# Kernel optimization log

Measured on AMD Instinct MI355X. Metric: run time of the kernel, lower is better.

## Reference

```python
import jax, jax.numpy as jnp
import numpy as np

N = 50000
E = 800000
IN_C, HID_C, OUT_C = 512, 128, 256


def setup_inputs() -> dict:
    key = jax.random.key(0)
    k1, k2, k3, k4, k5, k6 = jax.random.split(key, 6)
    x = jax.random.normal(k1, (N, IN_C), dtype=jnp.float32)
    edge_index = jax.random.randint(k2, (2, E), 0, N, dtype=jnp.int64)
    # Linear weights stored torch-style as [out, in]; bias per layer
    w1 = jax.random.normal(k3, (HID_C, IN_C), dtype=jnp.float32) * (1.0 / np.sqrt(IN_C))
    b1 = jax.random.normal(k4, (HID_C,), dtype=jnp.float32) * 0.02
    w2 = jax.random.normal(k5, (OUT_C, HID_C), dtype=jnp.float32) * (1.0 / np.sqrt(HID_C))
    b2 = jax.random.normal(k6, (OUT_C,), dtype=jnp.float32) * 0.02
    return {"x": x, "edge_index": edge_index, "w1": w1, "b1": b1, "w2": w2, "b2": b2}


def gcn_conv(x, edge_index, w, b):
    # x: [N, Cin], w: [Cout, Cin] (torch Linear layout), b: [Cout]
    h = x @ w.T                              # [N, Cout]
    src, dst = edge_index[0], edge_index[1]
    msgs = h[src]                            # gather: [E, Cout]
    agg = jax.ops.segment_sum(msgs, dst, num_segments=h.shape[0])  # scatter_add
    return agg + b


def reference(x, edge_index, w1, b1, w2, b2):
    h = gcn_conv(x, edge_index, w1, b1)
    h = jax.nn.relu(h)
    out = gcn_conv(h, edge_index, w2, b2)
    return out
```

## Files before the change

### kernel.cpp

```cpp
#include <hip/hip_runtime.h>

#define NN 50000
#define EE 800000
#define INC 512
#define HIDC 128
#define OUTC 256
#define CAP 64
#define OV_CAP 65536
#define BUILD_BLOCKS 192
#define BLK_PER_XCD (BUILD_BLOCKS / 8)
#define GRP_THREADS (BLK_PER_XCD * 256)
#define NCHUNK (EE / 16)
#define SLICE (NN / 8)
#define GB1 782

typedef __attribute__((ext_vector_type(8))) short bf16x8;
typedef __attribute__((ext_vector_type(4))) float f32x4;

__device__ __forceinline__ short f2bf(float f) {
    unsigned u = __float_as_uint(f);
    unsigned r = u + 0x7fff + ((u >> 16) & 1);
    return (short)(r >> 16);
}
__device__ __forceinline__ float bf2f(short s) {
    return __uint_as_float(((unsigned)(unsigned short)s) << 16);
}

template<bool IN_BF16, bool ADDBIAS, bool OUT_BF16>
__device__ __forceinline__ void gemm_core(
    const void* __restrict__ Av, const float* __restrict__ B,
    const float* __restrict__ bias, void* __restrict__ Cv,
    int M, int Nc, int K, int bx, int by,
    short As[64][72], short Bs[128][72])
{
    int tid = threadIdx.x;
    int lane = tid & 63, wave = tid >> 6;
    int row0 = bx * 64, col0 = by * 128;
    int wm = (wave & 1) * 32, wn = (wave >> 1) * 64;
    int l16 = lane & 15, quad = lane >> 4;

    f32x4 acc[2][4];
#pragma unroll
    for (int i = 0; i < 2; i++)
#pragma unroll
        for (int j = 0; j < 4; j++) acc[i][j] = {0.f, 0.f, 0.f, 0.f};

    for (int k0 = 0; k0 < K; k0 += 64) {
        if (IN_BF16) {
            const short* A = (const short*)Av;
#pragma unroll
            for (int w = 0; w < 2; w++) {
                int f = tid + w * 256;
                int rr = f >> 3, c8 = f & 7;
                int gr = row0 + rr;
                bf16x8 v = {0, 0, 0, 0, 0, 0, 0, 0};
                if (gr < M) v = *(const bf16x8*)&A[(long)gr * K + k0 + c8 * 8];
                *(bf16x8*)&As[rr][c8 * 8] = v;
            }
        } else {
            const float* A = (const float*)Av;
#pragma unroll
            for (int w = 0; w < 4; w++) {
                int f = tid + w * 256;
                int rr = f >> 4, c4 = f & 15;
                int gr = row0 + rr;
                float4 v = make_float4(0.f, 0.f, 0.f, 0.f);
                if (gr < M) v = *(const float4*)&A[(long)gr * K + k0 + c4 * 4];
                short4 s;
                s.x = f2bf(v.x); s.y = f2bf(v.y); s.z = f2bf(v.z); s.w = f2bf(v.w);
                *(short4*)&As[rr][c4 * 4] = s;
            }
        }
#pragma unroll
        for (int w = 0; w < 8; w++) {
            int f = tid + w * 256;
            int rr = f >> 4, c4 = f & 15;
            float4 v = *(const float4*)&B[(long)(col0 + rr) * K + k0 + c4 * 4];
            short4 s;
            s.x = f2bf(v.x); s.y = f2bf(v.y); s.z = f2bf(v.z); s.w = f2bf(v.w);
            *(short4*)&Bs[rr][c4 * 4] = s;
        }
        __syncthreads();

#pragma unroll
        for (int kk = 0; kk < 64; kk += 32) {
            bf16x8 af[2], bfr[4];
#pragma unroll
            for (int i = 0; i < 2; i++)
                af[i] = *(const bf16x8*)&As[wm + i * 16 + l16][kk + quad * 8];
#pragma unroll
            for (int j = 0; j < 4; j++)
                bfr[j] = *(const bf16x8*)&Bs[wn + j * 16 + l16][kk + quad * 8];
#pragma unroll
            for (int i = 0; i < 2; i++)
#pragma unroll
                for (int j = 0; j < 4; j++)
                    acc[i][j] = __builtin_amdgcn_mfma_f32_16x16x32_bf16(
                        af[i], bfr[j], acc[i][j], 0, 0, 0);
        }
        __syncthreads();
    }

#pragma unroll
    for (int i = 0; i < 2; i++) {
#pragma unroll
        for (int rr = 0; rr < 4; rr++) {
            int grow = row0 + wm + i * 16 + quad * 4 + rr;
            if (grow < M) {
#pragma unroll
                for (int j = 0; j < 4; j++) {
                    int gcol = col0 + wn + j * 16 + l16;
                    float v = acc[i][j][rr];
                    if (ADDBIAS) v += bias[gcol];
                    if (OUT_BF16)
                        ((short*)Cv)[(long)grow * Nc + gcol] = f2bf(v);
                    else
                        ((float*)Cv)[(long)grow * Nc + gcol] = v;
                }
            }
        }
    }
}

__global__ __launch_bounds__(256) void fat_build_gemm1(
    const int* __restrict__ ei, int* __restrict__ cnt,
    unsigned short* __restrict__ bucket, int* __restrict__ ovcnt,
    int* __restrict__ ovlist,
    const float* __restrict__ x, const float* __restrict__ w1,
    short* __restrict__ h)
{
    __shared__ short As[64][72];
    __shared__ short Bs[128][72];

    if (blockIdx.x < BUILD_BLOCKS) {
        int g = blockIdx.x & 7;
        int rank = blockIdx.x >> 3;
        int tig = rank * 256 + threadIdx.x;
        int lo = g * SLICE;
        for (int c = tig; c < NCHUNK; c += GRP_THREADS) {
            long base = (long)c * 16;
            int4 sv[4], dv[4];
#pragma unroll
            for (int q = 0; q < 4; q++) {
                sv[q] = *(const int4*)&ei[base + q * 4];
                dv[q] = *(const int4*)&ei[EE + base + q * 4];
            }
            const int* sp = (const int*)sv;
            const int* dp = (const int*)dv;
#pragma unroll
            for (int k = 0; k < 16; k++) {
                int dst = dp[k];
                if ((unsigned)(dst - lo) < SLICE) {
                    int src = sp[k];
                    int pos = atomicAdd(&cnt[dst], 1);
                    if (pos < CAP) bucket[(long)dst * CAP + pos] = (unsigned short)src;
                    else {
                        int o = atomicAdd(ovcnt, 1);
                        if (o < OV_CAP) { ovlist[o * 2] = src; ovlist[o * 2 + 1] = dst; }
                    }
                }
            }
        }
    } else {
        gemm_core<false, false, true>(x, w1, nullptr, h, NN, HIDC, INC,
                                      blockIdx.x - BUILD_BLOCKS, 0, As, Bs);
    }
}

__global__ __launch_bounds__(256) void gemm2_k(
    const short* __restrict__ r2, const float* __restrict__ w2,
    const float* __restrict__ b2, float* __restrict__ out)
{
    __shared__ short As[64][72];
    __shared__ short Bs[128][72];
    gemm_core<true, true, false>(r2, w2, b2, out, NN, OUTC, HIDC,
                                 blockIdx.x, blockIdx.y, As, Bs);
}

template<bool RELU>
__global__ __launch_bounds__(256) void gather_k(
    const short* __restrict__ hsrc, const unsigned short* __restrict__ bucket,
    const int* __restrict__ cnt, const float* __restrict__ bias,
    short* __restrict__ rout)
{
    int t = threadIdx.x;
    int node = blockIdx.x * 16 + (t >> 4);
    int c8 = t & 15;
    if (node >= NN) return;
    int m = cnt[node]; if (m > CAP) m = CAP;
    const unsigned short* bk = bucket + (long)node * CAP;
    float acc[8];
#pragma unroll
    for (int k = 0; k < 8; k++) acc[k] = 0.f;
    int j = 0;
    for (; j + 4 <= m; j += 4) {
        int s0 = bk[j], s1 = bk[j + 1], s2 = bk[j + 2], s3 = bk[j + 3];
        bf16x8 v0 = *(const bf16x8*)&hsrc[((long)s0 << 7) + c8 * 8];
        bf16x8 v1 = *(const bf16x8*)&hsrc[((long)s1 << 7) + c8 * 8];
        bf16x8 v2 = *(const bf16x8*)&hsrc[((long)s2 << 7) + c8 * 8];
        bf16x8 v3 = *(const bf16x8*)&hsrc[((long)s3 << 7) + c8 * 8];
#pragma unroll
        for (int k = 0; k < 8; k++)
            acc[k] += bf2f(v0[k]) + bf2f(v1[k]) + bf2f(v2[k]) + bf2f(v3[k]);
    }
    for (; j < m; j++) {
        int s0 = bk[j];
        bf16x8 v0 = *(const bf16x8*)&hsrc[((long)s0 << 7) + c8 * 8];
#pragma unroll
        for (int k = 0; k < 8; k++) acc[k] += bf2f(v0[k]);
    }
    bf16x8 o;
    if (RELU) {
#pragma unroll
        for (int k = 0; k < 8; k++)
            o[k] = f2bf(fmaxf(acc[k] + bias[c8 * 8 + k], 0.f));
    } else {
#pragma unroll
        for (int k = 0; k < 8; k++) o[k] = f2bf(acc[k]);
    }
    *(bf16x8*)&rout[((long)node << 7) + c8 * 8] = o;
}

__global__ __launch_bounds__(128) void ovfix1_k(
    const short* __restrict__ h, const float* __restrict__ b1,
    const unsigned short* __restrict__ bucket, const int* __restrict__ cnt,
    const int* __restrict__ ovcnt, const int* __restrict__ ovlist,
    short* __restrict__ r)
{
    int n = *ovcnt; if (n > OV_CAP) n = OV_CAP;
    int c = threadIdx.x;
    for (int i = 0; i < n; i++) {
        int dst = ovlist[i * 2 + 1];
        bool dup = false;
        for (int i2 = 0; i2 < i; i2++)
            if (ovlist[i2 * 2 + 1] == dst) { dup = true; break; }
        if (dup) continue;
        int m = cnt[dst]; if (m > CAP) m = CAP;
        const unsigned short* bk = bucket + (long)dst * CAP;
        float acc = 0.f;
        for (int j = 0; j < m; j++)
            acc += bf2f(h[(long)bk[j] * 128 + c]);
        for (int i2 = 0; i2 < n; i2++)
            if (ovlist[i2 * 2 + 1] == dst)
                acc += bf2f(h[(long)ovlist[i2 * 2] * 128 + c]);
        r[(long)dst * 128 + c] = f2bf(fmaxf(acc + b1[c], 0.f));
    }
}

__global__ __launch_bounds__(128) void ovfix2_k(
    const short* __restrict__ r, const unsigned short* __restrict__ bucket,
    const int* __restrict__ cnt, const int* __restrict__ ovcnt,
    const int* __restrict__ ovlist, short* __restrict__ r2)
{
    int n = *ovcnt; if (n > OV_CAP) n = OV_CAP;
    int c = threadIdx.x;
    for (int i = 0; i < n; i++) {
        int dst = ovlist[i * 2 + 1];
        bool dup = false;
        for (int i2 = 0; i2 < i; i2++)
            if (ovlist[i2 * 2 + 1] == dst) { dup = true; break; }
        if (dup) continue;
        int m = cnt[dst]; if (m > CAP) m = CAP;
        const unsigned short* bk = bucket + (long)dst * CAP;
        float acc = 0.f;
        for (int j = 0; j < m; j++)
            acc += bf2f(r[(long)bk[j] * 128 + c]);
        for (int i2 = 0; i2 < n; i2++)
            if (ovlist[i2 * 2 + 1] == dst)
                acc += bf2f(r[(long)ovlist[i2 * 2] * 128 + c]);
        r2[(long)dst * 128 + c] = f2bf(acc);
    }
}

extern "C" void kernel_launch(void* const* d_in, const int* in_sizes, int n_in,
                              void* d_out, int out_size, void* d_ws, size_t ws_size,
                              hipStream_t stream) {
    const float* x  = (const float*)d_in[0];
    const int*   ei = (const int*)d_in[1];
    const float* w1 = (const float*)d_in[2];
    const float* b1 = (const float*)d_in[3];
    const float* w2 = (const float*)d_in[4];
    const float* b2 = (const float*)d_in[5];
    float* out = (float*)d_out;

    char* ws = (char*)d_ws;
    size_t off = 0;
    short* h    = (short*)(ws + off); off += (size_t)NN * HIDC * 2;
    short* r    = (short*)(ws + off); off += (size_t)NN * HIDC * 2;
    short* r2   = (short*)(ws + off); off += (size_t)NN * HIDC * 2;
    unsigned short* bucket = (unsigned short*)(ws + off);
    off += (size_t)NN * CAP * 2;
    int* cnt    = (int*)(ws + off);   off += (size_t)NN * 4;
    int* ovcnt  = (int*)(ws + off);   off += 256;
    int* ovlist = (int*)(ws + off);   off += (size_t)OV_CAP * 2 * 4;

    hipMemsetAsync(cnt, 0, (size_t)NN * 4 + 4, stream);

    dim3 blk(256);

    fat_build_gemm1<<<dim3(BUILD_BLOCKS + GB1), blk, 0, stream>>>(
        ei, cnt, bucket, ovcnt, ovlist, x, w1, h);

    gather_k<true><<<dim3(3125), blk, 0, stream>>>(h, bucket, cnt, b1, r);
    ovfix1_k<<<dim3(1), dim3(128), 0, stream>>>(h, b1, bucket, cnt, ovcnt, ovlist, r);

    gather_k<false><<<dim3(3125), blk, 0, stream>>>(r, bucket, cnt, nullptr, r2);
    ovfix2_k<<<dim3(1), dim3(128), 0, stream>>>(r, bucket, cnt, ovcnt, ovlist, r2);

    gemm2_k<<<dim3(GB1, 2), blk, 0, stream>>>(r2, w2, b2, out);
}
```

Measured before the change: 329.6 us.

## Drop XCD-sliced edge bucketing and unroll gather loop to eight neighbors

```diff
diff --git a/kernel.cpp b/kernel.cpp
--- a/kernel.cpp
+++ b/kernel.cpp
@@ -7,11 +7,7 @@
 #define OUTC 256
 #define CAP 64
 #define OV_CAP 65536
-#define BUILD_BLOCKS 192
-#define BLK_PER_XCD (BUILD_BLOCKS / 8)
-#define GRP_THREADS (BLK_PER_XCD * 256)
-#define NCHUNK (EE / 16)
-#define SLICE (NN / 8)
+#define BUILD_BLOCKS 196
 #define GB1 782
 
 typedef __attribute__((ext_vector_type(8))) short bf16x8;
@@ -133,12 +129,9 @@
     __shared__ short Bs[128][72];
 
     if (blockIdx.x < BUILD_BLOCKS) {
-        int g = blockIdx.x & 7;
-        int rank = blockIdx.x >> 3;
-        int tig = rank * 256 + threadIdx.x;
-        int lo = g * SLICE;
-        for (int c = tig; c < NCHUNK; c += GRP_THREADS) {
-            long base = (long)c * 16;
+        int t = threadIdx.x;
+        long base = ((long)blockIdx.x * 256 + t) * 16;
+        if (base + 16 <= EE) {
             int4 sv[4], dv[4];
 #pragma unroll
             for (int q = 0; q < 4; q++) {
@@ -149,9 +142,19 @@
             const int* dp = (const int*)dv;
 #pragma unroll
             for (int k = 0; k < 16; k++) {
-                int dst = dp[k];
-                if ((unsigned)(dst - lo) < SLICE) {
-                    int src = sp[k];
+                int src = sp[k], dst = dp[k];
+                int pos = atomicAdd(&cnt[dst], 1);
+                if (pos < CAP) bucket[(long)dst * CAP + pos] = (unsigned short)src;
+                else {
+                    int o = atomicAdd(ovcnt, 1);
+                    if (o < OV_CAP) { ovlist[o * 2] = src; ovlist[o * 2 + 1] = dst; }
+                }
+            }
+        } else {
+            for (int k = 0; k < 16; k++) {
+                long e = base + k;
+                if (e < EE) {
+                    int src = ei[e], dst = ei[EE + e];
                     int pos = atomicAdd(&cnt[dst], 1);
                     if (pos < CAP) bucket[(long)dst * CAP + pos] = (unsigned short)src;
                     else {
@@ -193,15 +196,18 @@
 #pragma unroll
     for (int k = 0; k < 8; k++) acc[k] = 0.f;
     int j = 0;
-    for (; j + 4 <= m; j += 4) {
-        int s0 = bk[j], s1 = bk[j + 1], s2 = bk[j + 2], s3 = bk[j + 3];
-        bf16x8 v0 = *(const bf16x8*)&hsrc[((long)s0 << 7) + c8 * 8];
-        bf16x8 v1 = *(const bf16x8*)&hsrc[((long)s1 << 7) + c8 * 8];
-        bf16x8 v2 = *(const bf16x8*)&hsrc[((long)s2 << 7) + c8 * 8];
-        bf16x8 v3 = *(const bf16x8*)&hsrc[((long)s3 << 7) + c8 * 8];
-#pragma unroll
-        for (int k = 0; k < 8; k++)
-            acc[k] += bf2f(v0[k]) + bf2f(v1[k]) + bf2f(v2[k]) + bf2f(v3[k]);
+    for (; j + 8 <= m; j += 8) {
+        int s[8];
+#pragma unroll
+        for (int q = 0; q < 8; q++) s[q] = bk[j + q];
+        bf16x8 v[8];
+#pragma unroll
+        for (int q = 0; q < 8; q++)
+            v[q] = *(const bf16x8*)&hsrc[((long)s[q] << 7) + c8 * 8];
+#pragma unroll
+        for (int q = 0; q < 8; q++)
+#pragma unroll
+            for (int k = 0; k < 8; k++) acc[k] += bf2f(v[q][k]);
     }
     for (; j < m; j++) {
         int s0 = bk[j];
```

Result: faster. 306.7 us (-7.0%).
